# Performance work log

Measured on AMD Instinct MI355X. Metric: run time of the kernel, lower is better.

Reference implementation:

```python
import jax, jax.numpy as jnp
import numpy as np

IN_DIM, HIDDEN, OUT_DIM = 1433, 64, 7
N_NODES, N_EDGES = 100000, 1600000


def setup_inputs() -> dict:
    key = jax.random.key(0)
    ks = jax.random.split(key, 8)
    x = jax.random.normal(ks[0], (N_NODES, IN_DIM), dtype=jnp.float32)
    edge_index = jax.random.randint(ks[1], (2, N_EDGES), 0, N_NODES, dtype=jnp.int64)
    # Glorot-ish init for weights, zeros for biases (PyG GCNConv default)
    W1 = jax.random.normal(ks[2], (IN_DIM, HIDDEN), dtype=jnp.float32) / np.sqrt(IN_DIM)
    b1 = jnp.zeros((HIDDEN,), dtype=jnp.float32)
    W2 = jax.random.normal(ks[3], (HIDDEN, HIDDEN), dtype=jnp.float32) / np.sqrt(HIDDEN)
    b2 = jnp.zeros((HIDDEN,), dtype=jnp.float32)
    Wout = jax.random.normal(ks[4], (HIDDEN, OUT_DIM), dtype=jnp.float32) / np.sqrt(HIDDEN)
    bout = jnp.zeros((OUT_DIM,), dtype=jnp.float32)
    return {"x": x, "edge_index": edge_index, "W1": W1, "b1": b1,
            "W2": W2, "b2": b2, "Wout": Wout, "bout": bout}


def _gcn_conv(h, src, dst, norm, W, b, n_nodes):
    # GCNConv: h' = D^{-1/2} (A+I) D^{-1/2} (h W) + b
    h = h @ W                                   # [N, F_out]
    msg = h[src] * norm[:, None]                # gather + scale  [E+N, F_out]
    out = jax.ops.segment_sum(msg, dst, num_segments=n_nodes)  # scatter-add
    return out + b


def reference(x, edge_index, W1, b1, W2, b2, Wout, bout):
    n = x.shape[0]
    # add self-loops
    loops = jnp.arange(n, dtype=edge_index.dtype)
    src = jnp.concatenate([edge_index[0], loops])
    dst = jnp.concatenate([edge_index[1], loops])
    # symmetric normalization: deg counted at destination with unit weights
    deg = jax.ops.segment_sum(jnp.ones_like(src, dtype=x.dtype), dst, num_segments=n)
    dinv = jnp.where(deg > 0, jax.lax.rsqrt(deg), 0.0)
    norm = dinv[src] * dinv[dst]                # [E+N]

    h = _gcn_conv(x, src, dst, norm, W1, b1, n)
    h = jax.nn.relu(h)
    # dropout(p=0.5) is identity in eval mode
    h = _gcn_conv(h, src, dst, norm, W2, b2, n)
    h = jax.nn.relu(h)
    logits = h @ Wout + bout
    return jax.nn.softmax(logits, axis=1)
```

## Files before the change

kernel.cpp:

```cpp
#include <hip/hip_runtime.h>
#include <math.h>

#define IN_DIM 1433
#define HID 64
#define NCLS 7

__global__ void detect64_kernel(const int* __restrict__ ei, int* flag, int E) {
    int i = blockIdx.x * blockDim.x + threadIdx.x;
    if (i < 16384 && i < E) {
        if (ei[2 * i + 1] != 0) atomicOr(flag, 1);
    }
}

__device__ __forceinline__ int get_src(const int* ei, int e, int E, int is32) {
    return is32 ? ei[e] : ei[2 * e];
}
__device__ __forceinline__ int get_dst(const int* ei, int e, int E, int is32) {
    return is32 ? ei[E + e] : ei[2 * E + 2 * e];
}

__global__ void count_deg_kernel(const int* __restrict__ ei, const int* __restrict__ flagp,
                                 int* __restrict__ cnt, int E) {
    int e = blockIdx.x * blockDim.x + threadIdx.x;
    if (e >= E) return;
    int is32 = *flagp;
    atomicAdd(&cnt[get_dst(ei, e, E, is32)], 1);
}

__global__ void dinv_kernel(const int* __restrict__ cnt, float* __restrict__ dinv, int n) {
    int i = blockIdx.x * blockDim.x + threadIdx.x;
    if (i < n) dinv[i] = rsqrtf((float)(cnt[i] + 1));
}

__global__ __launch_bounds__(256) void scan_local(const int* __restrict__ in,
                                                  int* __restrict__ out,
                                                  int* __restrict__ bsum, int N) {
    int t = threadIdx.x;
    int base = blockIdx.x * 1024 + t * 4;
    int v0 = (base + 0) < N ? in[base + 0] : 0;
    int v1 = (base + 1) < N ? in[base + 1] : 0;
    int v2 = (base + 2) < N ? in[base + 2] : 0;
    int v3 = (base + 3) < N ? in[base + 3] : 0;
    int sum = v0 + v1 + v2 + v3;
    int lane = t & 63, w = t >> 6;
    int x = sum;
#pragma unroll
    for (int off = 1; off < 64; off <<= 1) {
        int y = __shfl_up(x, off);
        if (lane >= off) x += y;
    }
    __shared__ int ws[4];
    if (lane == 63) ws[w] = x;
    __syncthreads();
    int woff = 0;
#pragma unroll
    for (int i = 0; i < 4; ++i) if (i < w) woff += ws[i];
    int excl = woff + x - sum;
    if ((base + 0) < N) out[base + 0] = excl;
    if ((base + 1) < N) out[base + 1] = excl + v0;
    if ((base + 2) < N) out[base + 2] = excl + v0 + v1;
    if ((base + 3) < N) out[base + 3] = excl + v0 + v1 + v2;
    if (t == 255) bsum[blockIdx.x] = woff + x;
}

__global__ void scan_bsums(int* __restrict__ bsum, int nb) {
    int lane = threadIdx.x;
    int i0 = 2 * lane, i1 = 2 * lane + 1;
    int a = i0 < nb ? bsum[i0] : 0;
    int b = i1 < nb ? bsum[i1] : 0;
    int sum = a + b;
    int x = sum;
#pragma unroll
    for (int off = 1; off < 64; off <<= 1) {
        int y = __shfl_up(x, off);
        if (lane >= off) x += y;
    }
    int excl = x - sum;
    if (i0 < nb) bsum[i0] = excl;
    if (i1 < nb) bsum[i1] = excl + a;
}

__global__ void scan_add(int* __restrict__ row_ptr, int* __restrict__ cursor,
                         const int* __restrict__ bsum, int N) {
    int i = blockIdx.x * blockDim.x + threadIdx.x;
    if (i >= N) return;
    int v = row_ptr[i] + bsum[i >> 10];
    row_ptr[i] = v;
    cursor[i] = v;
}

__global__ void fill_kernel(const int* __restrict__ ei, const int* __restrict__ flagp,
                            const float* __restrict__ dinv, int* __restrict__ cursor,
                            int* __restrict__ col, float* __restrict__ wnrm, int E) {
    int e = blockIdx.x * blockDim.x + threadIdx.x;
    if (e >= E) return;
    int is32 = *flagp;
    int s = get_src(ei, e, E, is32);
    int d = get_dst(ei, e, E, is32);
    int pos = atomicAdd(&cursor[d], 1);
    col[pos] = s;
    wnrm[pos] = dinv[s];
}

#define BM 128
#define BN 64
#define BKK 32

__global__ __launch_bounds__(256) void gemm1_kernel(const float* __restrict__ x,
                                                    const float* __restrict__ W,
                                                    float* __restrict__ out, int N) {
    __shared__ float As[BKK][BM + 4];
    __shared__ float Bs[BKK][BN];
    const int tid = threadIdx.x;
    const int blockRow = blockIdx.x * BM;
    const int tr = tid >> 4;
    const int tc = tid & 15;
    const int kk = tid & 31;
    const int rg = tid >> 5;
    const int bc = tid & 63;
    const int br0 = tid >> 6;

    float acc[8][4];
#pragma unroll
    for (int i = 0; i < 8; ++i)
#pragma unroll
        for (int j = 0; j < 4; ++j) acc[i][j] = 0.f;

    for (int k0 = 0; k0 < IN_DIM; k0 += BKK) {
        const int gk = k0 + kk;
        const bool kok = gk < IN_DIM;
#pragma unroll
        for (int it = 0; it < 4; ++it) {
            int row = rg * 16 + it * 4;
            int gr = blockRow + row;
            float4 v;
            v.x = (kok && (gr + 0) < N) ? x[(size_t)(gr + 0) * IN_DIM + gk] : 0.f;
            v.y = (kok && (gr + 1) < N) ? x[(size_t)(gr + 1) * IN_DIM + gk] : 0.f;
            v.z = (kok && (gr + 2) < N) ? x[(size_t)(gr + 2) * IN_DIM + gk] : 0.f;
            v.w = (kok && (gr + 3) < N) ? x[(size_t)(gr + 3) * IN_DIM + gk] : 0.f;
            *(float4*)&As[kk][row] = v;
        }
#pragma unroll
        for (int i = 0; i < 8; ++i) {
            int r = br0 + i * 4;
            int gkb = k0 + r;
            Bs[r][bc] = (gkb < IN_DIM) ? W[gkb * BN + bc] : 0.f;
        }
        __syncthreads();
#pragma unroll
        for (int k = 0; k < BKK; ++k) {
            float4 a0 = *(const float4*)&As[k][tr * 8];
            float4 a1 = *(const float4*)&As[k][tr * 8 + 4];
            float4 bv = *(const float4*)&Bs[k][tc * 4];
            float av[8] = {a0.x, a0.y, a0.z, a0.w, a1.x, a1.y, a1.z, a1.w};
            float bw[4] = {bv.x, bv.y, bv.z, bv.w};
#pragma unroll
            for (int i = 0; i < 8; ++i)
#pragma unroll
                for (int j = 0; j < 4; ++j) acc[i][j] = fmaf(av[i], bw[j], acc[i][j]);
        }
        __syncthreads();
    }
#pragma unroll
    for (int i = 0; i < 8; ++i) {
        int gr = blockRow + tr * 8 + i;
        if (gr < N) {
            float4 v = make_float4(acc[i][0], acc[i][1], acc[i][2], acc[i][3]);
            *(float4*)&out[(size_t)gr * HID + tc * 4] = v;
        }
    }
}

__global__ __launch_bounds__(256) void agg_kernel(const int* __restrict__ row_ptr,
                                                  const int* __restrict__ cnt,
                                                  const int* __restrict__ col,
                                                  const float* __restrict__ wnrm,
                                                  const float* __restrict__ dinv,
                                                  const float* __restrict__ h,
                                                  const float* __restrict__ bias,
                                                  float* __restrict__ out, int N) {
    int node = blockIdx.x * 4 + (threadIdx.x >> 6);
    if (node >= N) return;
    int lane = threadIdx.x & 63;
    int g = lane >> 4;
    int q = lane & 15;
    int start = row_ptr[node];
    int end = start + cnt[node];

    float ax = 0.f, ay = 0.f, az = 0.f, aw = 0.f;
    for (int e0 = start; e0 < end; e0 += 8) {
        int ea = e0 + g;
        int eb = e0 + 4 + g;
        int sa = 0, sb = 0;
        float wa = 0.f, wb = 0.f;
        if (ea < end) { sa = col[ea]; wa = wnrm[ea]; }
        if (eb < end) { sb = col[eb]; wb = wnrm[eb]; }
        const float4 ha = *(const float4*)&h[(size_t)sa * HID + q * 4];
        const float4 hb = *(const float4*)&h[(size_t)sb * HID + q * 4];
        ax = fmaf(ha.x, wa, ax); ay = fmaf(ha.y, wa, ay);
        az = fmaf(ha.z, wa, az); aw = fmaf(ha.w, wa, aw);
        ax = fmaf(hb.x, wb, ax); ay = fmaf(hb.y, wb, ay);
        az = fmaf(hb.z, wb, az); aw = fmaf(hb.w, wb, aw);
    }
    ax += __shfl_xor(ax, 16); ay += __shfl_xor(ay, 16);
    az += __shfl_xor(az, 16); aw += __shfl_xor(aw, 16);
    ax += __shfl_xor(ax, 32); ay += __shfl_xor(ay, 32);
    az += __shfl_xor(az, 32); aw += __shfl_xor(aw, 32);

    if (g == 0) {
        float dn = dinv[node];
        const float4 hs = *(const float4*)&h[(size_t)node * HID + q * 4];
        const float4 bq = *(const float4*)&bias[q * 4];
        float4 r;
        r.x = fmaxf(fmaf(dn, fmaf(dn, hs.x, ax), bq.x), 0.f);
        r.y = fmaxf(fmaf(dn, fmaf(dn, hs.y, ay), bq.y), 0.f);
        r.z = fmaxf(fmaf(dn, fmaf(dn, hs.z, az), bq.z), 0.f);
        r.w = fmaxf(fmaf(dn, fmaf(dn, hs.w, aw), bq.w), 0.f);
        *(float4*)&out[(size_t)node * HID + q * 4] = r;
    }
}

__global__ __launch_bounds__(256) void gemm2_kernel(const float* __restrict__ h,
                                                    const float* __restrict__ W,
                                                    float* __restrict__ out, int n64) {
    __shared__ float Ws[HID * HID];
    for (int i = threadIdx.x; i < HID * HID; i += 256) Ws[i] = W[i];
    __syncthreads();
    int idx = blockIdx.x * blockDim.x + threadIdx.x;
    if (idx >= n64) return;
    int node = idx >> 6, c = idx & 63;
    const float* hrow = h + (size_t)node * HID;
    float acc = 0.f;
#pragma unroll 8
    for (int k = 0; k < HID; ++k) acc = fmaf(hrow[k], Ws[k * HID + c], acc);
    out[idx] = acc;
}

__global__ void out_kernel(const float* __restrict__ h2, const float* __restrict__ Wout,
                           const float* __restrict__ bout, float* __restrict__ out, int N) {
    int node = blockIdx.x * blockDim.x + threadIdx.x;
    if (node >= N) return;
    float hv[HID];
    const float4* hp = (const float4*)(h2 + (size_t)node * HID);
#pragma unroll
    for (int i = 0; i < HID / 4; ++i) {
        float4 v = hp[i];
        hv[i * 4 + 0] = v.x; hv[i * 4 + 1] = v.y; hv[i * 4 + 2] = v.z; hv[i * 4 + 3] = v.w;
    }
    float lg[NCLS];
#pragma unroll
    for (int j = 0; j < NCLS; ++j) lg[j] = bout[j];
#pragma unroll
    for (int k = 0; k < HID; ++k)
#pragma unroll
        for (int j = 0; j < NCLS; ++j) lg[j] = fmaf(hv[k], Wout[k * NCLS + j], lg[j]);
    float m = lg[0];
#pragma unroll
    for (int j = 1; j < NCLS; ++j) m = fmaxf(m, lg[j]);
    float s = 0.f;
#pragma unroll
    for (int j = 0; j < NCLS; ++j) { lg[j] = expf(lg[j] - m); s += lg[j]; }
    float inv = 1.f / s;
#pragma unroll
    for (int j = 0; j < NCLS; ++j) out[(size_t)node * NCLS + j] = lg[j] * inv;
}

extern "C" void kernel_launch(void* const* d_in, const int* in_sizes, int n_in,
                              void* d_out, int out_size, void* d_ws, size_t ws_size,
                              hipStream_t stream) {
    const float* x    = (const float*)d_in[0];
    const int*   ei   = (const int*)d_in[1];
    const float* W1   = (const float*)d_in[2];
    const float* b1   = (const float*)d_in[3];
    const float* W2   = (const float*)d_in[4];
    const float* b2   = (const float*)d_in[5];
    const float* Wout = (const float*)d_in[6];
    const float* bout = (const float*)d_in[7];
    float* out = (float*)d_out;

    const int N = in_sizes[0] / IN_DIM;
    const int E = in_sizes[1] / 2;
    const int n64 = N * HID;

    char* ws = (char*)d_ws;
    size_t off = 0;
    auto take = [&](size_t bytes) { char* p = ws + off; off = (off + bytes + 255) & ~(size_t)255; return p; };
    int*   cnt     = (int*)take((size_t)N * 4);
    float* dinv    = (float*)take((size_t)N * 4);
    int*   row_ptr = (int*)take((size_t)N * 4);
    int*   cursor  = (int*)take((size_t)N * 4);
    int*   bsum    = (int*)take(512);
    int*   flag    = (int*)take(256);
    int*   col     = (int*)take((size_t)E * 4);
    float* wnrm    = (float*)take((size_t)E * 4);
    float* P0      = (float*)take((size_t)n64 * 4);
    float* P1      = (float*)take((size_t)n64 * 4);

    hipMemsetAsync(cnt, 0, (size_t)N * sizeof(int), stream);
    hipMemsetAsync(flag, 0, sizeof(int), stream);
    detect64_kernel<<<64, 256, 0, stream>>>(ei, flag, E);
    count_deg_kernel<<<(E + 255) / 256, 256, 0, stream>>>(ei, flag, cnt, E);
    dinv_kernel<<<(N + 255) / 256, 256, 0, stream>>>(cnt, dinv, N);

    int nb = (N + 1023) / 1024;
    scan_local<<<nb, 256, 0, stream>>>(cnt, row_ptr, bsum, N);
    scan_bsums<<<1, 64, 0, stream>>>(bsum, nb);
    scan_add<<<(N + 255) / 256, 256, 0, stream>>>(row_ptr, cursor, bsum, N);
    fill_kernel<<<(E + 255) / 256, 256, 0, stream>>>(ei, flag, dinv, cursor, col, wnrm, E);

    gemm1_kernel<<<(N + BM - 1) / BM, 256, 0, stream>>>(x, W1, P0, N);
    agg_kernel<<<(N + 3) / 4, 256, 0, stream>>>(row_ptr, cnt, col, wnrm, dinv, P0, b1, P1, N);

    gemm2_kernel<<<(n64 + 255) / 256, 256, 0, stream>>>(P1, W2, P0, n64);
    agg_kernel<<<(N + 3) / 4, 256, 0, stream>>>(row_ptr, cnt, col, wnrm, dinv, P0, b2, P1, N);

    out_kernel<<<(N + 255) / 256, 256, 0, stream>>>(P1, Wout, bout, out, N);
}
```

Baseline: 1.337 ms.

## Use split-bf16 MFMA for both dense GEMMs instead of FP32 FMA

Replaces the shared-memory FP32 tiled GEMM for x@W1 and the naive per-element W2 GEMM with a single MFMA kernel. It splits fp32 into bf16 hi/lo parts and issues three bf16 MFMAs per product to keep near-fp32 accuracy. Weights are pre-split and transposed by a small conversion kernel, and the A operand is converted in registers straight from global memory without LDS staging. This targets the compute-bound FP32 FMA cost of the large GEMM, at the price of unaligned direct global loads of x (row stride 1433), uncoalesced scattered output stores, and slightly lower precision.

```diff
diff --git a/kernel.cpp b/kernel.cpp
--- a/kernel.cpp
+++ b/kernel.cpp
@@ -2,8 +2,12 @@
 #include <math.h>
 
 #define IN_DIM 1433
+#define KPAD1 1440
 #define HID 64
 #define NCLS 7
+
+typedef __attribute__((ext_vector_type(8))) short short8;
+typedef __attribute__((ext_vector_type(4))) float f32x4;
 
 __global__ void detect64_kernel(const int* __restrict__ ei, int* flag, int E) {
     int i = blockIdx.x * blockDim.x + threadIdx.x;
@@ -102,71 +106,97 @@
     wnrm[pos] = dinv[s];
 }
 
-#define BM 128
-#define BN 64
-#define BKK 32
-
-__global__ __launch_bounds__(256) void gemm1_kernel(const float* __restrict__ x,
-                                                    const float* __restrict__ W,
-                                                    float* __restrict__ out, int N) {
-    __shared__ float As[BKK][BM + 4];
-    __shared__ float Bs[BKK][BN];
+__global__ void convw_kernel(const float* __restrict__ W, short* __restrict__ Bh,
+                             short* __restrict__ Bl, int K, int KP, int ncol) {
+    int idx = blockIdx.x * blockDim.x + threadIdx.x;
+    if (idx >= ncol * KP) return;
+    int colc = idx / KP, k = idx - colc * KP;
+    float v = (k < K) ? W[(size_t)k * ncol + colc] : 0.f;
+    unsigned u = __float_as_uint(v);
+    float hif = __uint_as_float(u & 0xFFFF0000u);
+    float lof = v - hif;
+    Bh[idx] = (short)(u >> 16);
+    Bl[idx] = (short)(__float_as_uint(lof) >> 16);
+}
+
+template<int K, int KP>
+__global__ __launch_bounds__(256) void gemm_mfma(const float* __restrict__ x,
+                                                 const short* __restrict__ Bh,
+                                                 const short* __restrict__ Bl,
+                                                 float* __restrict__ out, int N) {
     const int tid = threadIdx.x;
-    const int blockRow = blockIdx.x * BM;
-    const int tr = tid >> 4;
-    const int tc = tid & 15;
-    const int kk = tid & 31;
-    const int rg = tid >> 5;
-    const int bc = tid & 63;
-    const int br0 = tid >> 6;
-
-    float acc[8][4];
-#pragma unroll
-    for (int i = 0; i < 8; ++i)
-#pragma unroll
-        for (int j = 0; j < 4; ++j) acc[i][j] = 0.f;
-
-    for (int k0 = 0; k0 < IN_DIM; k0 += BKK) {
-        const int gk = k0 + kk;
-        const bool kok = gk < IN_DIM;
-#pragma unroll
-        for (int it = 0; it < 4; ++it) {
-            int row = rg * 16 + it * 4;
-            int gr = blockRow + row;
-            float4 v;
-            v.x = (kok && (gr + 0) < N) ? x[(size_t)(gr + 0) * IN_DIM + gk] : 0.f;
-            v.y = (kok && (gr + 1) < N) ? x[(size_t)(gr + 1) * IN_DIM + gk] : 0.f;
-            v.z = (kok && (gr + 2) < N) ? x[(size_t)(gr + 2) * IN_DIM + gk] : 0.f;
-            v.w = (kok && (gr + 3) < N) ? x[(size_t)(gr + 3) * IN_DIM + gk] : 0.f;
-            *(float4*)&As[kk][row] = v;
-        }
-#pragma unroll
-        for (int i = 0; i < 8; ++i) {
-            int r = br0 + i * 4;
-            int gkb = k0 + r;
-            Bs[r][bc] = (gkb < IN_DIM) ? W[gkb * BN + bc] : 0.f;
-        }
-        __syncthreads();
-#pragma unroll
-        for (int k = 0; k < BKK; ++k) {
-            float4 a0 = *(const float4*)&As[k][tr * 8];
-            float4 a1 = *(const float4*)&As[k][tr * 8 + 4];
-            float4 bv = *(const float4*)&Bs[k][tc * 4];
-            float av[8] = {a0.x, a0.y, a0.z, a0.w, a1.x, a1.y, a1.z, a1.w};
-            float bw[4] = {bv.x, bv.y, bv.z, bv.w};
-#pragma unroll
-            for (int i = 0; i < 8; ++i)
-#pragma unroll
-                for (int j = 0; j < 4; ++j) acc[i][j] = fmaf(av[i], bw[j], acc[i][j]);
-        }
-        __syncthreads();
-    }
-#pragma unroll
-    for (int i = 0; i < 8; ++i) {
-        int gr = blockRow + tr * 8 + i;
-        if (gr < N) {
-            float4 v = make_float4(acc[i][0], acc[i][1], acc[i][2], acc[i][3]);
-            *(float4*)&out[(size_t)gr * HID + tc * 4] = v;
+    const int w = tid >> 6, lane = tid & 63;
+    const int q = lane >> 4, m16 = lane & 15;
+    const int blockRow = blockIdx.x * 128;
+
+    f32x4 acc[2][4];
+#pragma unroll
+    for (int i = 0; i < 2; ++i)
+#pragma unroll
+        for (int c = 0; c < 4; ++c) acc[i][c] = (f32x4)(0.f);
+
+    const int row0 = blockRow + 16 * (2 * w + 0) + m16;
+    const int row1 = blockRow + 16 * (2 * w + 1) + m16;
+    const float* a0p = x + (size_t)min(row0, N - 1) * K;
+    const float* a1p = x + (size_t)min(row1, N - 1) * K;
+
+    const int nchunk = KP / 32;
+    for (int c = 0; c < nchunk; ++c) {
+        const int k0 = c * 32 + q * 8;
+        float av0[8], av1[8];
+        if (k0 + 8 <= K) {
+            __builtin_memcpy(&av0[0], a0p + k0, 16);
+            __builtin_memcpy(&av0[4], a0p + k0 + 4, 16);
+            __builtin_memcpy(&av1[0], a1p + k0, 16);
+            __builtin_memcpy(&av1[4], a1p + k0 + 4, 16);
+        } else {
+#pragma unroll
+            for (int j = 0; j < 8; ++j) {
+                int k = k0 + j;
+                av0[j] = (k < K) ? a0p[k] : 0.f;
+                av1[j] = (k < K) ? a1p[k] : 0.f;
+            }
+        }
+        short8 ah0, al0, ah1, al1;
+#pragma unroll
+        for (int j = 0; j < 8; ++j) {
+            unsigned u0 = __float_as_uint(av0[j]);
+            float lo0 = av0[j] - __uint_as_float(u0 & 0xFFFF0000u);
+            ah0[j] = (short)(u0 >> 16);
+            al0[j] = (short)(__float_as_uint(lo0) >> 16);
+            unsigned u1 = __float_as_uint(av1[j]);
+            float lo1 = av1[j] - __uint_as_float(u1 & 0xFFFF0000u);
+            ah1[j] = (short)(u1 >> 16);
+            al1[j] = (short)(__float_as_uint(lo1) >> 16);
+        }
+        short8 bh[4], bl[4];
+#pragma unroll
+        for (int ct = 0; ct < 4; ++ct) {
+            size_t boff = (size_t)(16 * ct + m16) * KP + k0;
+            __builtin_memcpy(&bh[ct], Bh + boff, 16);
+            __builtin_memcpy(&bl[ct], Bl + boff, 16);
+        }
+#pragma unroll
+        for (int ct = 0; ct < 4; ++ct) {
+            acc[0][ct] = __builtin_amdgcn_mfma_f32_16x16x32_bf16(ah0, bh[ct], acc[0][ct], 0, 0, 0);
+            acc[0][ct] = __builtin_amdgcn_mfma_f32_16x16x32_bf16(ah0, bl[ct], acc[0][ct], 0, 0, 0);
+            acc[0][ct] = __builtin_amdgcn_mfma_f32_16x16x32_bf16(al0, bh[ct], acc[0][ct], 0, 0, 0);
+            acc[1][ct] = __builtin_amdgcn_mfma_f32_16x16x32_bf16(ah1, bh[ct], acc[1][ct], 0, 0, 0);
+            acc[1][ct] = __builtin_amdgcn_mfma_f32_16x16x32_bf16(ah1, bl[ct], acc[1][ct], 0, 0, 0);
+            acc[1][ct] = __builtin_amdgcn_mfma_f32_16x16x32_bf16(al1, bh[ct], acc[1][ct], 0, 0, 0);
+        }
+    }
+#pragma unroll
+    for (int i = 0; i < 2; ++i) {
+        int rbase = blockRow + 16 * (2 * w + i) + q * 4;
+#pragma unroll
+        for (int r = 0; r < 4; ++r) {
+            int row = rbase + r;
+            if (row < N) {
+#pragma unroll
+                for (int ct = 0; ct < 4; ++ct)
+                    out[(size_t)row * HID + 16 * ct + m16] = acc[i][ct][r];
+            }
         }
     }
 }
@@ -220,22 +250,6 @@
     }
 }
 
-__global__ __launch_bounds__(256) void gemm2_kernel(const float* __restrict__ h,
-                                                    const float* __restrict__ W,
-                                                    float* __restrict__ out, int n64) {
-    __shared__ float Ws[HID * HID];
-    for (int i = threadIdx.x; i < HID * HID; i += 256) Ws[i] = W[i];
-    __syncthreads();
-    int idx = blockIdx.x * blockDim.x + threadIdx.x;
-    if (idx >= n64) return;
-    int node = idx >> 6, c = idx & 63;
-    const float* hrow = h + (size_t)node * HID;
-    float acc = 0.f;
-#pragma unroll 8
-    for (int k = 0; k < HID; ++k) acc = fmaf(hrow[k], Ws[k * HID + c], acc);
-    out[idx] = acc;
-}
-
 __global__ void out_kernel(const float* __restrict__ h2, const float* __restrict__ Wout,
                            const float* __restrict__ bout, float* __restrict__ out, int N) {
     int node = blockIdx.x * blockDim.x + threadIdx.x;
@@ -295,6 +309,10 @@
     float* wnrm    = (float*)take((size_t)E * 4);
     float* P0      = (float*)take((size_t)n64 * 4);
     float* P1      = (float*)take((size_t)n64 * 4);
+    short* W1h     = (short*)take((size_t)HID * KPAD1 * 2);
+    short* W1l     = (short*)take((size_t)HID * KPAD1 * 2);
+    short* W2h     = (short*)take((size_t)HID * HID * 2);
+    short* W2l     = (short*)take((size_t)HID * HID * 2);
 
     hipMemsetAsync(cnt, 0, (size_t)N * sizeof(int), stream);
     hipMemsetAsync(flag, 0, sizeof(int), stream);
@@ -308,10 +326,14 @@
     scan_add<<<(N + 255) / 256, 256, 0, stream>>>(row_ptr, cursor, bsum, N);
     fill_kernel<<<(E + 255) / 256, 256, 0, stream>>>(ei, flag, dinv, cursor, col, wnrm, E);
 
-    gemm1_kernel<<<(N + BM - 1) / BM, 256, 0, stream>>>(x, W1, P0, N);
+    convw_kernel<<<(HID * KPAD1 + 255) / 256, 256, 0, stream>>>(W1, W1h, W1l, IN_DIM, KPAD1, HID);
+    convw_kernel<<<(HID * HID + 255) / 256, 256, 0, stream>>>(W2, W2h, W2l, HID, HID, HID);
+
+    const int gblocks = (N + 127) / 128;
+    gemm_mfma<IN_DIM, KPAD1><<<gblocks, 256, 0, stream>>>(x, W1h, W1l, P0, N);
     agg_kernel<<<(N + 3) / 4, 256, 0, stream>>>(row_ptr, cnt, col, wnrm, dinv, P0, b1, P1, N);
 
-    gemm2_kernel<<<(n64 + 255) / 256, 256, 0, stream>>>(P1, W2, P0, n64);
+    gemm_mfma<HID, HID><<<gblocks, 256, 0, stream>>>(P1, W2h, W2l, P0, N);
     agg_kernel<<<(N + 3) / 4, 256, 0, stream>>>(row_ptr, cnt, col, wnrm, dinv, P0, b2, P1, N);
 
     out_kernel<<<(N + 255) / 256, 256, 0, stream>>>(P1, Wout, bout, out, N);
```

Measured after the change: 1.253 ms. -6.2%, faster.
